# Kernel tuning notes

Measured on AMD Instinct MI355X. Metric: run time of the kernel, lower is better.

## Reference

```python
import jax, jax.numpy as jnp
import numpy as np

WIN = 9  # window_size from init


def _box_filter_3d(x, k):
    """Separable normalized box filter over the 3 spatial dims of NCDHW x.
    Mathematically identical to a dense k^3 mean filter with SAME padding."""
    c = x.shape[1]
    pad = k // 2
    for axis in range(3):
        kshape = [1, 1, 1]
        kshape[axis] = k
        kern = jnp.ones((c, 1, *kshape), x.dtype) / k  # depthwise, normalized per-axis
        padding = [(pad, pad) if a == axis else (0, 0) for a in range(3)]
        x = jax.lax.conv_general_dilated(
            x, kern, window_strides=(1, 1, 1), padding=padding,
            dimension_numbers=('NCDHW', 'OIDHW', 'NCDHW'),
            feature_group_count=c)
    return x


def setup_inputs() -> dict:
    key = jax.random.key(0)
    k1, k2 = jax.random.split(key)
    shape = (1, 1, 192, 192, 192)
    pred = jax.random.uniform(k1, shape, dtype=jnp.float32)
    target = jax.random.uniform(k2, shape, dtype=jnp.float32)
    return {"pred": pred, "target": target}


def reference(pred, target):
    Ii, Ji = target, pred
    # local means of I, J, I^2, J^2, IJ via one grouped (5-channel) box filter
    all_five = jnp.concatenate([Ii, Ji, Ii * Ii, Ji * Ji, Ii * Ji], axis=1)
    f = _box_filter_3d(all_five, WIN)
    mu1, mu2 = f[:, 0:1], f[:, 1:2]
    conv_I2, conv_J2, conv_IJ = f[:, 2:3], f[:, 3:4], f[:, 4:5]
    sigma1_sq = conv_I2 - mu1 * mu1
    sigma2_sq = conv_J2 - mu2 * mu2
    sigma12 = conv_IJ - mu1 * mu2
    eps = jnp.finfo(sigma12.dtype).eps
    cc = sigma12 * sigma12 / (sigma1_sq * sigma2_sq + eps)
    return 1.0 - jnp.mean(cc)
```

## Files before the change

### kernel.cpp

```cpp
#include <hip/hip_runtime.h>
#include <hip/hip_bf16.h>

#define SDIM 192
#define S2 (SDIM*SDIM)
#define S3 ((size_t)SDIM*S2)
#define NCH 5
#define RAD 4

#define STRH 8
#define RROW 16
#define RQU 224
#define WSTR 96
#define NSTRIP (SDIM/STRH)
#define SQQ(Q) ((Q) + ((Q) >> 3))

#define KB_THR 128
#define KB_KBC 4
#define KB_POSB (S2/(KB_THR*KB_KBC))
#define KB_DCH 12
#define KB_NDC (SDIM/KB_DCH)
#define KB_GRID (KB_POSB*KB_NDC)
#define NPART KB_GRID

__device__ __forceinline__ unsigned packbf(float lo, float hi) {
    __hip_bfloat162 h2 = __float22bfloat162_rn(make_float2(lo, hi));
    unsigned u; __builtin_memcpy(&u, &h2, 4); return u;
}
__device__ __forceinline__ float ulo(unsigned u) { return __uint_as_float(u << 16); }
__device__ __forceinline__ float uhi(unsigned u) { return __uint_as_float(u & 0xffff0000u); }

__global__ __launch_bounds__(256) void ka_wh(const float* __restrict__ pred,
                                             const float* __restrict__ tgt,
                                             unsigned* __restrict__ BU) {
    const int b = blockIdx.x;
    const int strip = b % NSTRIP;
    const int d = b / NSTRIP;
    const int h0 = strip * STRH;
    const size_t dbase = (size_t)d * S2;
    const int t = threadIdx.x;

    __shared__ unsigned IJ[RROW][RQU];
    __shared__ unsigned wfU[NCH][RROW][WSTR];

    if (t < RROW * 8) {
        const int r = t >> 3, p = t & 7;
        const int col = (p < 4) ? p : (216 + p);
        IJ[r][col] = 0u;
    }
    const float4* tg4 = (const float4*)tgt;
    const float4* pr4 = (const float4*)pred;
#pragma unroll
    for (int it = 0; it < 3; ++it) {
        const int u = t + 256 * it;
        const int r = u / 48, q = u % 48;
        const int hh = h0 - RAD + r;
        float4 vi = make_float4(0.f, 0.f, 0.f, 0.f), vj = vi;
        if (hh >= 0 && hh < SDIM) {
            const size_t gi = (dbase + (size_t)hh * SDIM) / 4 + q;
            vi = tg4[gi]; vj = pr4[gi];
        }
        uint4 w;
        w.x = packbf(vi.x, vj.x); w.y = packbf(vi.y, vj.y);
        w.z = packbf(vi.z, vj.z); w.w = packbf(vi.w, vj.w);
        *(uint4*)&IJ[r][4 * SQQ(q + 1)] = w;
    }
    __syncthreads();

#pragma unroll
    for (int it = 0; it < 3; ++it) {
        const int u = t + 256 * it;
        const int row = u / 48, cu = u % 48;
        const uint4 a  = *(const uint4*)&IJ[row][4 * SQQ(cu)];
        const uint4 bq = *(const uint4*)&IJ[row][4 * SQQ(cu + 1)];
        const uint4 cq = *(const uint4*)&IJ[row][4 * SQQ(cu + 2)];
        unsigned raw[12] = {a.x, a.y, a.z, a.w, bq.x, bq.y, bq.z, bq.w,
                            cq.x, cq.y, cq.z, cq.w};
        float fi[12], fj[12];
#pragma unroll
        for (int k = 0; k < 12; ++k) { fi[k] = ulo(raw[k]); fj[k] = uhi(raw[k]); }

#define W4(CH, EXPR) { \
        float pv[12]; \
        _Pragma("unroll") for (int k = 0; k < 12; ++k) pv[k] = (EXPR); \
        float s0 = 0.f; \
        _Pragma("unroll") for (int k = 0; k < 9; ++k) s0 += pv[k]; \
        const float s1 = s0 - pv[0] + pv[9]; \
        const float s2 = s1 - pv[1] + pv[10]; \
        const float s3 = s2 - pv[2] + pv[11]; \
        uint2 o; o.x = packbf(s0, s1); o.y = packbf(s2, s3); \
        *(uint2*)&wfU[CH][row][2 * cu] = o; }

        W4(0, fi[k])
        W4(1, fj[k])
        W4(2, fi[k] * fi[k])
        W4(3, fj[k] * fj[k])
        W4(4, fi[k] * fj[k])
#undef W4
    }
    __syncthreads();

#pragma unroll
    for (int it = 0; it < 2; ++it) {
        const int col = t + 256 * it;
        if (col < NCH * 96) {
            const int c = col / 96, wp = col % 96;
            float lo[RROW], hi[RROW];
#pragma unroll
            for (int r = 0; r < RROW; ++r) {
                const unsigned v = wfU[c][r][wp];
                lo[r] = ulo(v); hi[r] = uhi(v);
            }
            float slo = 0.f, shi = 0.f;
#pragma unroll
            for (int r = 0; r < 9; ++r) { slo += lo[r]; shi += hi[r]; }
            unsigned* dst = BU + (size_t)c * (S3 / 2) + (dbase + (size_t)h0 * SDIM) / 2 + wp;
            dst[0] = packbf(slo, shi);
#pragma unroll
            for (int hr = 1; hr < STRH; ++hr) {
                slo += lo[hr + 8] - lo[hr - 1];
                shi += hi[hr + 8] - hi[hr - 1];
                dst[hr * (SDIM / 2)] = packbf(slo, shi);
            }
        }
    }
}

#define SLICE2(s, OP) { const size_t sb = ((size_t)(s) * S2 + pos0) >> 2; \
    _Pragma("unroll") for (int c = 0; c < NCH; ++c) { \
        const uint2 v = B2[(size_t)c * (S3 >> 2) + sb]; \
        z[c][0] OP ulo(v.x); z[c][1] OP uhi(v.x); \
        z[c][2] OP ulo(v.y); z[c][3] OP uhi(v.y); } }

__global__ __launch_bounds__(KB_THR) void kb_d_cc(const unsigned* __restrict__ BU,
                                                  float* __restrict__ partials) {
    const int bid = blockIdx.x;
    const int dc = bid / KB_POSB;
    const int pb = bid % KB_POSB;
    const int d0 = dc * KB_DCH;
    const int pos0 = pb * (KB_THR * KB_KBC) + threadIdx.x * KB_KBC;
    const uint2* B2 = (const uint2*)BU;

    float z[NCH][KB_KBC];
#pragma unroll
    for (int c = 0; c < NCH; ++c)
#pragma unroll
        for (int i = 0; i < KB_KBC; ++i) z[c][i] = 0.f;

#pragma unroll
    for (int dd = -RAD; dd <= RAD; ++dd) {
        const int s = d0 + dd;
        if (s >= 0 && s < SDIM) SLICE2(s, +=)
    }

    const float inv = 1.0f / 729.0f;
    const float eps = 1.1920929e-07f;
    float acc = 0.f;

#pragma unroll
    for (int k = 0; k < KB_DCH; ++k) {
        const int d = d0 + k;
#pragma unroll
        for (int i = 0; i < KB_KBC; ++i) {
            const float mu1 = z[0][i] * inv;
            const float mu2 = z[1][i] * inv;
            const float sg1 = z[2][i] * inv - mu1 * mu1;
            const float sg2 = z[3][i] * inv - mu2 * mu2;
            const float s12 = z[4][i] * inv - mu1 * mu2;
            acc += (s12 * s12) * __builtin_amdgcn_rcpf(sg1 * sg2 + eps);
        }
        const int da = d + RAD + 1;
        const int ds = d - RAD;
        if (da < SDIM) SLICE2(da, +=)
        if (ds >= 0)   SLICE2(ds, -=)
    }

    __shared__ float red[KB_THR];
    red[threadIdx.x] = acc;
    __syncthreads();
#pragma unroll
    for (int o = KB_THR / 2; o > 0; o >>= 1) {
        if (threadIdx.x < o) red[threadIdx.x] += red[threadIdx.x + o];
        __syncthreads();
    }
    if (threadIdx.x == 0) partials[bid] = red[0];
}

__global__ __launch_bounds__(256) void k4_finalize(const float* __restrict__ partials,
                                                   float* __restrict__ out) {
    __shared__ float sm[256];
    float s = 0.f;
    for (int i = threadIdx.x; i < NPART; i += 256) s += partials[i];
    sm[threadIdx.x] = s;
    __syncthreads();
#pragma unroll
    for (int o = 128; o > 0; o >>= 1) {
        if (threadIdx.x < o) sm[threadIdx.x] += sm[threadIdx.x + o];
        __syncthreads();
    }
    if (threadIdx.x == 0) out[0] = 1.0f - sm[0] / (float)((size_t)SDIM * S2);
}

extern "C" void kernel_launch(void* const* d_in, const int* in_sizes, int n_in,
                              void* d_out, int out_size, void* d_ws, size_t ws_size,
                              hipStream_t stream) {
    const float* pred = (const float*)d_in[0];
    const float* tgt  = (const float*)d_in[1];
    float* out = (float*)d_out;

    const size_t b_bytes = (size_t)NCH * S3 * sizeof(__hip_bfloat16);
    const size_t b_pad = (b_bytes + 255) & ~(size_t)255;

    unsigned* BU = (unsigned*)d_ws;
    float* partials = (float*)((char*)d_ws + b_pad);

    ka_wh<<<SDIM * NSTRIP, 256, 0, stream>>>(pred, tgt, BU);
    kb_d_cc<<<KB_GRID, KB_THR, 0, stream>>>(BU, partials);
    k4_finalize<<<1, 256, 0, stream>>>(partials, out);
}
```

Before: 76.85 us.

## Load W-window inputs directly from global, shrink depth-pass blocks, use wave shuffle reduce

The W/H pass no longer stages packed bf16 pred/target rows in shared memory. Each thread now reads its three overlapping float4 chunks straight from global memory, which drops one barrier and the bf16 rounding of the inputs, but fetches each element about three times (mostly served from cache). The H sliding sum is written with two-wide float vectors. The depth pass drops to 64-thread blocks covering 8 slices each, giving more blocks but more halo re-reads, and its shared-memory tree reduction is replaced by a single-wavefront shuffle reduction.

```diff
diff --git a/kernel.cpp b/kernel.cpp
--- a/kernel.cpp
+++ b/kernel.cpp
@@ -9,18 +9,18 @@
 
 #define STRH 8
 #define RROW 16
-#define RQU 224
 #define WSTR 96
 #define NSTRIP (SDIM/STRH)
-#define SQQ(Q) ((Q) + ((Q) >> 3))
-
-#define KB_THR 128
+
+#define KB_THR 64
 #define KB_KBC 4
 #define KB_POSB (S2/(KB_THR*KB_KBC))
-#define KB_DCH 12
+#define KB_DCH 8
 #define KB_NDC (SDIM/KB_DCH)
 #define KB_GRID (KB_POSB*KB_NDC)
 #define NPART KB_GRID
+
+typedef float v2f __attribute__((ext_vector_type(2)));
 
 __device__ __forceinline__ unsigned packbf(float lo, float hi) {
     __hip_bfloat162 h2 = __float22bfloat162_rn(make_float2(lo, hi));
@@ -39,45 +39,35 @@
     const size_t dbase = (size_t)d * S2;
     const int t = threadIdx.x;
 
-    __shared__ unsigned IJ[RROW][RQU];
     __shared__ unsigned wfU[NCH][RROW][WSTR];
 
-    if (t < RROW * 8) {
-        const int r = t >> 3, p = t & 7;
-        const int col = (p < 4) ? p : (216 + p);
-        IJ[r][col] = 0u;
-    }
     const float4* tg4 = (const float4*)tgt;
     const float4* pr4 = (const float4*)pred;
-#pragma unroll
-    for (int it = 0; it < 3; ++it) {
-        const int u = t + 256 * it;
-        const int r = u / 48, q = u % 48;
-        const int hh = h0 - RAD + r;
-        float4 vi = make_float4(0.f, 0.f, 0.f, 0.f), vj = vi;
-        if (hh >= 0 && hh < SDIM) {
-            const size_t gi = (dbase + (size_t)hh * SDIM) / 4 + q;
-            vi = tg4[gi]; vj = pr4[gi];
-        }
-        uint4 w;
-        w.x = packbf(vi.x, vj.x); w.y = packbf(vi.y, vj.y);
-        w.z = packbf(vi.z, vj.z); w.w = packbf(vi.w, vj.w);
-        *(uint4*)&IJ[r][4 * SQQ(q + 1)] = w;
-    }
-    __syncthreads();
 
 #pragma unroll
     for (int it = 0; it < 3; ++it) {
         const int u = t + 256 * it;
         const int row = u / 48, cu = u % 48;
-        const uint4 a  = *(const uint4*)&IJ[row][4 * SQQ(cu)];
-        const uint4 bq = *(const uint4*)&IJ[row][4 * SQQ(cu + 1)];
-        const uint4 cq = *(const uint4*)&IJ[row][4 * SQQ(cu + 2)];
-        unsigned raw[12] = {a.x, a.y, a.z, a.w, bq.x, bq.y, bq.z, bq.w,
-                            cq.x, cq.y, cq.z, cq.w};
-        float fi[12], fj[12];
-#pragma unroll
-        for (int k = 0; k < 12; ++k) { fi[k] = ulo(raw[k]); fj[k] = uhi(raw[k]); }
+        const int hh = h0 - RAD + row;
+        const bool hok = (hh >= 0) && (hh < SDIM);
+        const size_t rb4 = (dbase + (size_t)(hok ? hh : 0) * SDIM) >> 2;
+        float4 qi[3], qj[3];
+#pragma unroll
+        for (int s = 0; s < 3; ++s) {
+            const int q = cu - 1 + s;
+            const bool ok = hok && (q >= 0) && (q < 48);
+            if (ok) { qi[s] = tg4[rb4 + q]; qj[s] = pr4[rb4 + q]; }
+            else {
+                qi[s] = make_float4(0.f, 0.f, 0.f, 0.f);
+                qj[s] = make_float4(0.f, 0.f, 0.f, 0.f);
+            }
+        }
+        const float fi[12] = {qi[0].x, qi[0].y, qi[0].z, qi[0].w,
+                              qi[1].x, qi[1].y, qi[1].z, qi[1].w,
+                              qi[2].x, qi[2].y, qi[2].z, qi[2].w};
+        const float fj[12] = {qj[0].x, qj[0].y, qj[0].z, qj[0].w,
+                              qj[1].x, qj[1].y, qj[1].z, qj[1].w,
+                              qj[2].x, qj[2].y, qj[2].z, qj[2].w};
 
 #define W4(CH, EXPR) { \
         float pv[12]; \
@@ -104,22 +94,21 @@
         const int col = t + 256 * it;
         if (col < NCH * 96) {
             const int c = col / 96, wp = col % 96;
-            float lo[RROW], hi[RROW];
+            v2f vh[RROW];
 #pragma unroll
             for (int r = 0; r < RROW; ++r) {
                 const unsigned v = wfU[c][r][wp];
-                lo[r] = ulo(v); hi[r] = uhi(v);
+                vh[r] = (v2f){ulo(v), uhi(v)};
             }
-            float slo = 0.f, shi = 0.f;
-#pragma unroll
-            for (int r = 0; r < 9; ++r) { slo += lo[r]; shi += hi[r]; }
+            v2f s = vh[0];
+#pragma unroll
+            for (int r = 1; r < 9; ++r) s += vh[r];
             unsigned* dst = BU + (size_t)c * (S3 / 2) + (dbase + (size_t)h0 * SDIM) / 2 + wp;
-            dst[0] = packbf(slo, shi);
+            dst[0] = packbf(s.x, s.y);
 #pragma unroll
             for (int hr = 1; hr < STRH; ++hr) {
-                slo += lo[hr + 8] - lo[hr - 1];
-                shi += hi[hr + 8] - hi[hr - 1];
-                dst[hr * (SDIM / 2)] = packbf(slo, shi);
+                s += vh[hr + 8] - vh[hr - 1];
+                dst[hr * (SDIM / 2)] = packbf(s.x, s.y);
             }
         }
     }
@@ -174,15 +163,10 @@
         if (ds >= 0)   SLICE2(ds, -=)
     }
 
-    __shared__ float red[KB_THR];
-    red[threadIdx.x] = acc;
-    __syncthreads();
-#pragma unroll
-    for (int o = KB_THR / 2; o > 0; o >>= 1) {
-        if (threadIdx.x < o) red[threadIdx.x] += red[threadIdx.x + o];
-        __syncthreads();
-    }
-    if (threadIdx.x == 0) partials[bid] = red[0];
+#pragma unroll
+    for (int off = 32; off > 0; off >>= 1)
+        acc += __shfl_down(acc, off, 64);
+    if (threadIdx.x == 0) partials[bid] = acc;
 }
 
 __global__ __launch_bounds__(256) void k4_finalize(const float* __restrict__ partials,
```

Result: slower. 79.92 us (+4.0%).
